# Kernel optimization log

Hardware: AMD Instinct MI355X
Metric: run time of the kernel (lower is better)

The kernel has to match this reference:

```python
import jax, jax.numpy as jnp
import numpy as np

B, T, C = 2, 4096, 768
NH = 12
HD = C // NH  # 64


def setup_inputs() -> dict:
    key = jax.random.key(0)
    k0, k1, k2, k3, k4 = jax.random.split(key, 5)
    x = jax.random.normal(k0, (B, T, C), dtype=jnp.float32)
    # parameters (stored as [in, out] for x @ W)
    w_attn = jax.random.normal(k1, (C, 3 * C), dtype=jnp.float32) * 0.02
    b_attn = jnp.zeros((3 * C,), dtype=jnp.float32)
    w_proj = jax.random.normal(k2, (C, C), dtype=jnp.float32) * 0.02
    b_proj = jnp.zeros((C,), dtype=jnp.float32)
    return {"x": x, "w_attn": w_attn, "b_attn": b_attn, "w_proj": w_proj, "b_proj": b_proj}


def reference(x, w_attn, b_attn, w_proj, b_proj):
    Bv, Tv, Cv = x.shape
    qkv = x @ w_attn + b_attn  # (B,T,3C)
    q, k, v = jnp.split(qkv, 3, axis=2)
    # (B, NH, T, HD)
    q = q.reshape(Bv, Tv, NH, HD).transpose(0, 2, 1, 3)
    k = k.reshape(Bv, Tv, NH, HD).transpose(0, 2, 1, 3)
    v = v.reshape(Bv, Tv, NH, HD).transpose(0, 2, 1, 3)
    att = jnp.einsum('bhqd,bhkd->bhqk', q, k) / jnp.sqrt(jnp.float32(HD))
    causal = jnp.tril(jnp.ones((Tv, Tv), dtype=bool))  # mask buffer slice
    att = jnp.where(causal[None, None, :, :], att, jnp.float32(-jnp.inf))
    att = jax.nn.softmax(att, axis=-1)
    y = jnp.einsum('bhqk,bhkd->bhqd', att, v)
    y = y.transpose(0, 2, 1, 3).reshape(Bv, Tv, Cv)
    y = y @ w_proj + b_proj
    return y
```

## Files before the change

kernel.cpp:

```cpp
#include <hip/hip_runtime.h>

typedef __bf16 bf16;
typedef float f32x4 __attribute__((ext_vector_type(4)));
typedef bf16 bf16x8v __attribute__((ext_vector_type(8)));
typedef bf16 bf16x4v __attribute__((ext_vector_type(4)));

#define MFMA_BF16(a, b, c) __builtin_amdgcn_mfma_f32_16x16x32_bf16((a), (b), (c), 0, 0, 0)

__device__ __forceinline__ void async16(const bf16* g, bf16* l) {
  __builtin_amdgcn_global_load_lds(
      (const __attribute__((address_space(1))) void*)g,
      (__attribute__((address_space(3))) void*)l, 16, 0, 0);
}

__global__ __launch_bounds__(256) void prep_kernel(
    const float* __restrict__ x, bf16* __restrict__ xb,
    const float* __restrict__ w_attn, bf16* __restrict__ wt_attn,
    const float* __restrict__ w_proj, bf16* __restrict__ wt_proj) {
  __shared__ float tile[32][33];
  const int b = blockIdx.x;
  if (b < 3072) {
    int i = b * 256 + threadIdx.x;
    const float4* p = (const float4*)x + (size_t)i * 2;
    float4 a = p[0], c = p[1];
    bf16x8v o;
    o[0] = (bf16)a.x; o[1] = (bf16)a.y; o[2] = (bf16)a.z; o[3] = (bf16)a.w;
    o[4] = (bf16)c.x; o[5] = (bf16)c.y; o[6] = (bf16)c.z; o[7] = (bf16)c.w;
    ((bf16x8v*)xb)[i] = o;
    return;
  }
  const float* in;
  bf16* out;
  int Ccols, bidx;
  if (b < 4800) {
    in = w_attn; out = wt_attn; Ccols = 2304; bidx = b - 3072;
  } else {
    in = w_proj; out = wt_proj; Ccols = 768; bidx = b - 4800;
  }
  const int R = 768;
  const int gx = Ccols / 32;
  const int c0 = (bidx % gx) * 32, r0 = (bidx / gx) * 32;
  const int tx = threadIdx.x & 31;
  const int ty = threadIdx.x >> 5;
#pragma unroll
  for (int i = 0; i < 4; ++i) {
    int r = ty + i * 8;
    tile[r][tx] = in[(size_t)(r0 + r) * Ccols + c0 + tx];
  }
  __syncthreads();
#pragma unroll
  for (int i = 0; i < 4; ++i) {
    int c = ty + i * 8;
    out[(size_t)(c0 + c) * R + r0 + tx] = (bf16)tile[tx][c];
  }
}

__global__ __launch_bounds__(256) void transpose_bf16_kernel(
    const bf16* __restrict__ in, bf16* __restrict__ out, int R, int Ccols) {
  __shared__ bf16 tile[32][33];
  const bf16* inp = in + (size_t)blockIdx.z * R * Ccols;
  bf16* outp = out + (size_t)blockIdx.z * R * Ccols;
  int c0 = blockIdx.x * 32, r0 = blockIdx.y * 32;
  int tx = threadIdx.x & 31;
  int ty = threadIdx.x >> 5;
#pragma unroll
  for (int i = 0; i < 4; ++i) {
    int r = ty + i * 8;
    tile[r][tx] = inp[(size_t)(r0 + r) * Ccols + c0 + tx];
  }
  __syncthreads();
#pragma unroll
  for (int i = 0; i < 4; ++i) {
    int c = ty + i * 8;
    outp[(size_t)(c0 + c) * R + r0 + tx] = tile[tx][c];
  }
}

template <int MODE, int GX>
__global__ __launch_bounds__(256) void gemm_kernel(
    const bf16* __restrict__ A, const bf16* __restrict__ Bt,
    const float* __restrict__ bias, int N, float* __restrict__ outf,
    bf16* __restrict__ qo, bf16* __restrict__ ko, bf16* __restrict__ vo) {
  constexpr int Kdim = 768;
  __shared__ __align__(16) bf16 As[128][64];
  __shared__ __align__(16) bf16 Bs[128][64];
  const int tid = threadIdx.x;
  const int lane = tid & 63;
  const int wave = tid >> 6;
  const int wm = (wave >> 1) * 64, wn = (wave & 1) * 64;
  const int id = blockIdx.x;
  const int xcd = id & 7, j = id >> 3;
  const int m0 = (xcd * 8 + (j & 7)) * 128;
  const int n0 = (j >> 3) * 128;
  const int l15 = lane & 15, q4 = lane >> 4;
  const int swz = l15 & 7;

  f32x4 acc[4][4] = {};

  const int gr = lane >> 3;
  const int sj = (lane & 7) ^ gr;

  for (int k0 = 0; k0 < Kdim; k0 += 64) {
#pragma unroll
    for (int c = 0; c < 4; ++c) {
      const int r0 = wave * 32 + c * 8;
      async16(A + (size_t)(m0 + r0 + gr) * Kdim + k0 + sj * 8, &As[r0][0]);
      async16(Bt + (size_t)(n0 + r0 + gr) * Kdim + k0 + sj * 8, &Bs[r0][0]);
    }
    __syncthreads();
#pragma unroll
    for (int ks = 0; ks < 2; ++ks) {
      bf16x8v af[4], bfg[4];
#pragma unroll
      for (int i = 0; i < 4; ++i)
        af[i] =
            *(const bf16x8v*)&As[wm + i * 16 + l15][((ks * 4 + q4) ^ swz) * 8];
#pragma unroll
      for (int i = 0; i < 4; ++i)
        bfg[i] =
            *(const bf16x8v*)&Bs[wn + i * 16 + l15][((ks * 4 + q4) ^ swz) * 8];
#pragma unroll
      for (int mi = 0; mi < 4; ++mi)
#pragma unroll
        for (int ni = 0; ni < 4; ++ni)
          acc[mi][ni] = MFMA_BF16(af[mi], bfg[ni], acc[mi][ni]);
    }
    __syncthreads();
  }

#pragma unroll
  for (int mi = 0; mi < 4; ++mi) {
#pragma unroll
    for (int ni = 0; ni < 4; ++ni) {
      int col = n0 + wn + ni * 16 + l15;
      float bv = bias[col];
#pragma unroll
      for (int r = 0; r < 4; ++r) {
        int row = m0 + wm + mi * 16 + q4 * 4 + r;
        float val = acc[mi][ni][r] + bv;
        if (MODE == 0) {
          outf[(size_t)row * N + col] = val;
        } else {
          int sel = col / 768;
          int cc = col - sel * 768;
          int h = cc >> 6, d = cc & 63;
          int b = row >> 12, t = row & 4095;
          bf16* dst = sel == 0 ? qo : (sel == 1 ? ko : vo);
          dst[((size_t)(b * 12 + h) * 4096 + t) * 64 + d] = (bf16)val;
        }
      }
    }
  }
}

__global__ __launch_bounds__(512, 6) void attn_kernel(
    const bf16* __restrict__ q, const bf16* __restrict__ k,
    const bf16* __restrict__ vt, bf16* __restrict__ y) {
  __shared__ __align__(16) bf16 Kb[2][64][64];
  __shared__ __align__(16) bf16 Vb[2][64][64];
  __shared__ __align__(16) bf16 Ps[8][16][64];
  const int tid = threadIdx.x;
  const int lane = tid & 63, wave = tid >> 6;
  const int l15 = lane & 15, q4 = lane >> 4;
  const int swz = l15 & 7;
  const int id = blockIdx.x;
  const int bh = id % 24;
  const int p = id / 24;
  const int rs = (wave < 4) ? ((63 - p) * 64 + wave * 16)
                            : (p * 64 + (wave - 4) * 16);
  const int hb = bh % 12, bb = bh / 12;

  const int gr = lane >> 3;
  const int sj = (lane & 7) ^ gr;
  const bf16* kgbase = k + (size_t)bh * 4096 * 64;
  const bf16* vgbase = vt + (size_t)bh * 64 * 4096;

  bf16x8v ones;
#pragma unroll
  for (int j = 0; j < 8; ++j) ones[j] = (bf16)1.0f;

  bf16x8v qf[2];
  {
    const bf16* qrow = q + ((size_t)bh * 4096 + rs + l15) * 64 + q4 * 8;
#pragma unroll
    for (int ks = 0; ks < 2; ++ks) {
      bf16x8v t8 = *(const bf16x8v*)(qrow + ks * 32);
#pragma unroll
      for (int j = 0; j < 8; ++j) t8[j] = (bf16)((float)t8[j] * 0.18033688f);
      qf[ks] = t8;
    }
  }

  f32x4 o[4] = {};
  f32x4 ol = {};

  auto stage = [&](int kt, int buf) {
    const int t0k = kt * 64;
    async16(kgbase + (size_t)(t0k + wave * 8 + gr) * 64 + sj * 8,
            &Kb[buf][wave * 8][0]);
    async16(vgbase + (size_t)(wave * 8 + gr) * 4096 + t0k + sj * 8,
            &Vb[buf][wave * 8][0]);
  };

  auto sm_full = [&](f32x4 (&s)[4]) {
#pragma unroll
    for (int ni = 0; ni < 4; ++ni)
#pragma unroll
      for (int r = 0; r < 4; ++r)
        s[ni][r] = __builtin_amdgcn_exp2f(s[ni][r] - 28.8539008f);
  };
  auto sm_mask = [&](f32x4 (&s)[4], int lim) {
#pragma unroll
    for (int ni = 0; ni < 4; ++ni)
#pragma unroll
      for (int r = 0; r < 4; ++r)
        s[ni][r] = (ni * 16 + q4 * 4 + r <= lim)
                       ? __builtin_amdgcn_exp2f(s[ni][r] - 28.8539008f)
                       : 0.0f;
  };
  auto pwrite = [&](const f32x4 (&s)[4]) {
#pragma unroll
    for (int ni = 0; ni < 4; ++ni) {
      bf16x4v pv4;
#pragma unroll
      for (int e = 0; e < 4; ++e) pv4[e] = (bf16)s[ni][e];
      const int jb = ni * 2 + (q4 >> 1);
      *(bf16x4v*)&Ps[wave][l15][((jb ^ (l15 & 7)) * 8) + (q4 & 1) * 4] = pv4;
    }
  };

  const int ktmax = 64 - p;
  stage(0, 0);

  for (int kt = 0; kt < ktmax; ++kt) {
    const int buf = kt & 1;
    __syncthreads();
    if (kt + 1 < ktmax) stage(kt + 1, buf ^ 1);
    const int t0 = kt * 64;

    if (t0 <= rs + 15) {
      f32x4 s[4] = {};
      __builtin_amdgcn_s_setprio(1);
#pragma unroll
      for (int ni = 0; ni < 4; ++ni) {
#pragma unroll
        for (int ks = 0; ks < 2; ++ks) {
          bf16x8v kf = *(const bf16x8v*)&Kb[buf][ni * 16 + l15]
                                           [((ks * 4 + q4) ^ swz) * 8];
          s[ni] = MFMA_BF16(kf, qf[ks], s[ni]);
        }
      }
      __builtin_amdgcn_s_setprio(0);

      if (t0 + 63 <= rs) sm_full(s); else sm_mask(s, rs + l15 - t0);
      pwrite(s);

      bf16x8v pf[2];
#pragma unroll
      for (int ks = 0; ks < 2; ++ks)
        pf[ks] = *(const bf16x8v*)&Ps[wave][l15][((ks * 4 + q4) ^ swz) * 8];

      __builtin_amdgcn_s_setprio(1);
#pragma unroll
      for (int d4 = 0; d4 < 4; ++d4) {
#pragma unroll
        for (int ks = 0; ks < 2; ++ks) {
          bf16x8v vf = *(const bf16x8v*)&Vb[buf][d4 * 16 + l15]
                                           [((ks * 4 + q4) ^ swz) * 8];
          o[d4] = MFMA_BF16(pf[ks], vf, o[d4]);
        }
      }
#pragma unroll
      for (int ks = 0; ks < 2; ++ks) ol = MFMA_BF16(pf[ks], ones, ol);
      __builtin_amdgcn_s_setprio(0);
    }
  }

#pragma unroll
  for (int d4 = 0; d4 < 4; ++d4)
#pragma unroll
    for (int r = 0; r < 4; ++r) {
      int row = rs + q4 * 4 + r;
      y[((size_t)(bb * 4096 + row)) * 768 + hb * 64 + d4 * 16 + l15] =
          (bf16)(o[d4][r] / ol[r]);
    }
}

extern "C" void kernel_launch(void* const* d_in, const int* in_sizes, int n_in,
                              void* d_out, int out_size, void* d_ws,
                              size_t ws_size, hipStream_t stream) {
  const float* x = (const float*)d_in[0];
  const float* w_attn = (const float*)d_in[1];
  const float* b_attn = (const float*)d_in[2];
  const float* w_proj = (const float*)d_in[3];
  const float* b_proj = (const float*)d_in[4];
  float* out = (float*)d_out;

  char* ws = (char*)d_ws;
  size_t off = 0;
  auto carve = [&](size_t elems) {
    char* p = ws + off;
    off += ((elems * sizeof(bf16) + 255) & ~(size_t)255);
    return (bf16*)p;
  };
  bf16* xb = carve((size_t)8192 * 768);
  bf16* wt_attn = carve((size_t)2304 * 768);
  bf16* wt_proj = carve((size_t)768 * 768);
  bf16* qb = carve((size_t)24 * 4096 * 64);
  bf16* kb = carve((size_t)24 * 4096 * 64);
  bf16* vb = carve((size_t)24 * 4096 * 64);
  bf16* vtb = xb;
  bf16* yb = vb;

  prep_kernel<<<5376, 256, 0, stream>>>(x, xb, w_attn, wt_attn, w_proj,
                                        wt_proj);
  gemm_kernel<1, 18><<<1152, 256, 0, stream>>>(xb, wt_attn, b_attn, 2304,
                                               nullptr, qb, kb, vb);
  transpose_bf16_kernel<<<dim3(64 / 32, 4096 / 32, 24), 256, 0, stream>>>(
      vb, vtb, 4096, 64);
  attn_kernel<<<dim3(768), 512, 0, stream>>>(qb, kb, vtb, yb);
  gemm_kernel<0, 6><<<384, 256, 0, stream>>>(yb, wt_proj, b_proj, 768, out,
                                             nullptr, nullptr, nullptr);
}
```

Baseline: 237.6 us.

## Use 64-row tiles for projection GEMM and remap attention blocks across XCDs

```diff
diff --git a/kernel.cpp b/kernel.cpp
--- a/kernel.cpp
+++ b/kernel.cpp
@@ -76,43 +76,54 @@
   }
 }
 
-template <int MODE, int GX>
+template <int MODE, int BM>
 __global__ __launch_bounds__(256) void gemm_kernel(
     const bf16* __restrict__ A, const bf16* __restrict__ Bt,
     const float* __restrict__ bias, int N, float* __restrict__ outf,
     bf16* __restrict__ qo, bf16* __restrict__ ko, bf16* __restrict__ vo) {
   constexpr int Kdim = 768;
-  __shared__ __align__(16) bf16 As[128][64];
+  constexpr int MI = BM / 32;
+  __shared__ __align__(16) bf16 As[BM][64];
   __shared__ __align__(16) bf16 Bs[128][64];
   const int tid = threadIdx.x;
   const int lane = tid & 63;
   const int wave = tid >> 6;
-  const int wm = (wave >> 1) * 64, wn = (wave & 1) * 64;
+  const int wm = (wave >> 1) * (BM / 2), wn = (wave & 1) * 64;
   const int id = blockIdx.x;
   const int xcd = id & 7, j = id >> 3;
-  const int m0 = (xcd * 8 + (j & 7)) * 128;
-  const int n0 = (j >> 3) * 128;
+  int m0, n0;
+  if (BM == 128) {
+    m0 = (xcd * 8 + (j & 7)) * 128;
+    n0 = (j >> 3) * 128;
+  } else {
+    m0 = (xcd * 16 + (j & 15)) * 64;
+    n0 = (j >> 4) * 128;
+  }
   const int l15 = lane & 15, q4 = lane >> 4;
   const int swz = l15 & 7;
 
-  f32x4 acc[4][4] = {};
+  f32x4 acc[MI][4] = {};
 
   const int gr = lane >> 3;
   const int sj = (lane & 7) ^ gr;
 
   for (int k0 = 0; k0 < Kdim; k0 += 64) {
 #pragma unroll
+    for (int c = 0; c < BM / 32; ++c) {
+      const int r0 = wave * (BM / 4) + c * 8;
+      async16(A + (size_t)(m0 + r0 + gr) * Kdim + k0 + sj * 8, &As[r0][0]);
+    }
+#pragma unroll
     for (int c = 0; c < 4; ++c) {
       const int r0 = wave * 32 + c * 8;
-      async16(A + (size_t)(m0 + r0 + gr) * Kdim + k0 + sj * 8, &As[r0][0]);
       async16(Bt + (size_t)(n0 + r0 + gr) * Kdim + k0 + sj * 8, &Bs[r0][0]);
     }
     __syncthreads();
 #pragma unroll
     for (int ks = 0; ks < 2; ++ks) {
-      bf16x8v af[4], bfg[4];
-#pragma unroll
-      for (int i = 0; i < 4; ++i)
+      bf16x8v af[MI], bfg[4];
+#pragma unroll
+      for (int i = 0; i < MI; ++i)
         af[i] =
             *(const bf16x8v*)&As[wm + i * 16 + l15][((ks * 4 + q4) ^ swz) * 8];
 #pragma unroll
@@ -120,7 +131,7 @@
         bfg[i] =
             *(const bf16x8v*)&Bs[wn + i * 16 + l15][((ks * 4 + q4) ^ swz) * 8];
 #pragma unroll
-      for (int mi = 0; mi < 4; ++mi)
+      for (int mi = 0; mi < MI; ++mi)
 #pragma unroll
         for (int ni = 0; ni < 4; ++ni)
           acc[mi][ni] = MFMA_BF16(af[mi], bfg[ni], acc[mi][ni]);
@@ -129,7 +140,7 @@
   }
 
 #pragma unroll
-  for (int mi = 0; mi < 4; ++mi) {
+  for (int mi = 0; mi < MI; ++mi) {
 #pragma unroll
     for (int ni = 0; ni < 4; ++ni) {
       int col = n0 + wn + ni * 16 + l15;
@@ -164,8 +175,13 @@
   const int l15 = lane & 15, q4 = lane >> 4;
   const int swz = l15 & 7;
   const int id = blockIdx.x;
-  const int bh = id % 24;
-  const int p = id / 24;
+  const int r_ = id & 255, s_ = id >> 8;
+  const int m_ = r_ >> 3, rho = r_ & 7;
+  const int b_ = (m_ + s_) % 3;
+  const int bh = rho + 8 * b_;
+  const int p = (b_ == 0) ? m_
+              : (b_ == 1) ? ((m_ < 16) ? 30 - 2 * m_ : 63 - 2 * m_)
+                          : ((m_ + 16) & 31);
   const int rs = (wave < 4) ? ((63 - p) * 64 + wave * 16)
                             : (p * 64 + (wave - 4) * 16);
   const int hb = bh % 12, bb = bh / 12;
@@ -314,11 +330,11 @@
 
   prep_kernel<<<5376, 256, 0, stream>>>(x, xb, w_attn, wt_attn, w_proj,
                                         wt_proj);
-  gemm_kernel<1, 18><<<1152, 256, 0, stream>>>(xb, wt_attn, b_attn, 2304,
-                                               nullptr, qb, kb, vb);
+  gemm_kernel<1, 128><<<1152, 256, 0, stream>>>(xb, wt_attn, b_attn, 2304,
+                                                nullptr, qb, kb, vb);
   transpose_bf16_kernel<<<dim3(64 / 32, 4096 / 32, 24), 256, 0, stream>>>(
       vb, vtb, 4096, 64);
   attn_kernel<<<dim3(768), 512, 0, stream>>>(qb, kb, vtb, yb);
-  gemm_kernel<0, 6><<<384, 256, 0, stream>>>(yb, wt_proj, b_proj, 768, out,
-                                             nullptr, nullptr, nullptr);
-}
+  gemm_kernel<0, 64><<<768, 256, 0, stream>>>(yb, wt_proj, b_proj, 768, out,
+                                              nullptr, nullptr, nullptr);
+}
```

Measured after the change: 241.5 us. Within noise of the previous version (+1.7%).
